# Performance work log

Hardware: AMD Instinct MI355X
Metric: run time of the kernel (lower is better)

Reference implementation:

```python
import jax, jax.numpy as jnp
import numpy as np

WS = 7            # window size (fixed by RelativeEmbedding default)
EMBED = 96
HEADS = 3
BATCH = 64
SIDE = 56         # height = width = sqrt(3136)
NEG_INF = float('-inf')


def _rel_bias_from_table(b_np):
    # Faithful reproduction of RelativeEmbedding.__init__ indexing quirks:
    # x = arange(1, ws+1, 1/ws) -> 49 floats; diffs truncated toward zero (.int())
    x = np.arange(1, WS + 1, 1.0 / WS, dtype=np.float32)
    xi = np.trunc(x[None, :] - x[:, None]).astype(np.int64)  # in [-6, 6]
    y = np.concatenate([np.arange(1, WS + 1)] * WS)
    yi = (y[None, :] - y[:, None]).astype(np.int64)          # in [-6, 6]
    n = 2 * WS - 1  # 13; emulate torch negative indexing with mod
    return b_np[xi % n, yi % n]  # (49, 49)


def _shift_masks():
    m = WS * (WS // 2)  # 21
    row_mask = np.zeros((WS * WS, WS * WS), dtype=np.float32)
    row_mask[-m:, :-m] = NEG_INF
    row_mask[:-m, -m:] = NEG_INF
    # rearrange '(r w1) (c w2) -> (w1 r) (w2 c)'
    col_mask = row_mask.reshape(WS, WS, WS, WS).transpose(1, 0, 3, 2).reshape(WS * WS, WS * WS)
    return jnp.asarray(row_mask), jnp.asarray(col_mask)


def setup_inputs() -> dict:
    key = jax.random.key(0)
    k1, k2, k3, k4, k5, k6 = jax.random.split(key, 6)
    x = jax.random.normal(k1, (BATCH, SIDE * SIDE, EMBED), dtype=jnp.float32)
    w1 = jax.random.normal(k2, (EMBED, 3 * EMBED), dtype=jnp.float32) * 0.02
    b1 = jnp.zeros((3 * EMBED,), dtype=jnp.float32)
    w2 = jax.random.normal(k3, (EMBED, EMBED), dtype=jnp.float32) * 0.02
    b2 = jnp.zeros((EMBED,), dtype=jnp.float32)
    b_table = np.asarray(jax.random.normal(k4, (2 * WS - 1, 2 * WS - 1), dtype=jnp.float32))
    rel_bias = jnp.asarray(_rel_bias_from_table(b_table))  # (49, 49), non-trainable
    return {"x": x, "w1": w1, "b1": b1, "w2": w2, "b2": b2, "rel_bias": rel_bias}


def reference(x, w1, b1, w2, b2, rel_bias):
    Bz, N, C = x.shape
    side = SIDE
    H = HEADS
    E = C // H          # head dim = 32
    nh = side // WS     # 8 windows per side

    qkv = x @ w1 + b1                                   # (B, N, 3C)
    # 'b (h w) (c K) -> b h w c K' with K=3 fastest-varying
    qkv = qkv.reshape(Bz, side, side, C, 3)
    # shifted-window roll; note (-7)//2 == -4 in Python (faithful to source)
    qkv = jnp.roll(qkv, ((-WS) // 2, (-WS) // 2), axis=(1, 2))
    # 'b (h m1) (w m2) (H E) K -> b H h w (m1 m2) E K'
    qkv = qkv.reshape(Bz, nh, WS, nh, WS, H, E, 3)
    qkv = qkv.transpose(0, 5, 1, 3, 2, 4, 6, 7).reshape(Bz, H, nh, nh, WS * WS, E, 3)
    q, k, v = qkv[..., 0], qkv[..., 1], qkv[..., 2]

    scale = jnp.sqrt(jnp.float32(E))
    att = jnp.einsum('bHhwme,bHhwne->bHhwmn', q, k) / scale  # (B,H,8,8,49,49)
    att = att + rel_bias

    row_mask, col_mask = _shift_masks()
    att = att.at[:, :, -1, :].add(row_mask)   # last window row
    att = att.at[:, :, :, -1].add(col_mask)   # last window column

    p = jax.nn.softmax(att, axis=-1)
    out = jnp.einsum('bHhwmn,bHhwne->bHhwme', p, v)          # (B,H,8,8,49,32)

    # 'b H h w (m1 m2) E -> b (h m1) (w m2) (H E)'
    out = out.reshape(Bz, H, nh, nh, WS, WS, E)
    out = out.transpose(0, 2, 4, 3, 5, 1, 6).reshape(Bz, side, side, C)
    # reverse roll uses +(7//2) == +3 (faithful asymmetry in the source)
    out = jnp.roll(out, (WS // 2, WS // 2), axis=(1, 2))
    out = out.reshape(Bz, N, C)
    return out @ w2 + b2
```

## Files before the change

kernel.cpp:

```cpp
#include <hip/hip_runtime.h>
#include <hip/hip_fp16.h>

typedef _Float16 half8_t __attribute__((ext_vector_type(8)));
typedef _Float16 half4_t __attribute__((ext_vector_type(4)));
typedef float f32x4 __attribute__((ext_vector_type(4)));
typedef unsigned int u32x4 __attribute__((ext_vector_type(4)));

#define WS_W2T 55296
#define WS_B1P 73728
#define WS_TBL 74880

__global__ __launch_bounds__(256) void swin_prep_kernel(
    const float* __restrict__ w1, const float* __restrict__ b1,
    const float* __restrict__ w2, const float* __restrict__ relb,
    _Float16* __restrict__ w1T, _Float16* __restrict__ w2T,
    float* __restrict__ b1p, float* __restrict__ tblP)
{
    int idx = blockIdx.x * 256 + threadIdx.x;
    const float L2E = 1.4426950408889634f;
    const float qs2 = 0.17677669529663687f * L2E;
    if (idx < 27648) {
        int jp = idx / 96, k = idx % 96;
        float v;
        if (jp < 96) {
            int f = jp >> 4, m = jp & 15;
            int cq = (f >> 1) * 32 + (m >> 2) * 8 + (f & 1) * 4 + (m & 3);
            v = w1[k * 288 + cq * 3] * qs2;
        } else {
            int jo = (jp % 96) * 3 + (jp / 96);
            v = w1[k * 288 + jo];
        }
        w1T[idx] = (_Float16)v;
    } else if (idx < 36864) {
        int i2 = idx - 27648;
        int n = i2 / 96, k = i2 % 96;
        w2T[i2] = (_Float16)w2[k * 96 + n];
    } else if (idx < 37152) {
        int jp = idx - 36864;
        float v = b1[(jp % 96) * 3 + (jp / 96)];
        if (jp < 96) v *= qs2;
        b1p[jp] = v;
    } else if (idx < 53536) {
        int t = idx - 37152;
        int vv = t >> 12, q = (t >> 6) & 63, c = t & 63;
        int i = c >> 4, m = c & 15;
        int k = (i >> 1) * 32 + (m >> 2) * 8 + (i & 1) * 4 + (m & 3);
        float val = -1e30f;
        if (q < 49 && k < 49) {
            val = relb[q * 49 + k] * L2E;
            if ((vv & 1) && ((q >= 28) != (k >= 28))) val = -1e30f;
            if ((vv & 2) && (((q % 7) >= 4) != ((k % 7) >= 4))) val = -1e30f;
        }
        tblP[t] = val;
    }
}

__device__ __forceinline__ unsigned int pack2h(float a, float b) {
    union { _Float16 h[2]; unsigned int u; } p;
    p.h[0] = (_Float16)a; p.h[1] = (_Float16)b;
    return p.u;
}

__global__ __launch_bounds__(256, 4) void swin_attn_kernel(
    const float* __restrict__ x,
    const _Float16* __restrict__ w1T,
    const _Float16* __restrict__ w2T,
    const float* __restrict__ b1p,
    const float* __restrict__ b2,
    const float* __restrict__ tblP,
    float* __restrict__ out)
{
    __shared__ __align__(16) char smem[27136];
    _Float16* Kb = (_Float16*)smem;
    _Float16* Vt = (_Float16*)(smem + 13312);
    _Float16* Xs = Kb;

    const int tid = threadIdx.x;
    const int wv = tid >> 6, lane = tid & 63;
    const int lr = lane & 15, lg = lane >> 4;

    const int gid = blockIdx.x;
    const int b = gid >> 6, wh = (gid >> 3) & 7, ww = gid & 7;
    const f32x4 fz = {0.f, 0.f, 0.f, 0.f};

    {
        const int p = tid >> 2, sub = tid & 3;
        const float* xrow = nullptr;
        if (p < 49) {
            const int m1 = p / 7, m2 = p % 7;
            int rr = wh * 7 + m1 + 4; if (rr >= 56) rr -= 56;
            int cc = ww * 7 + m2 + 4; if (cc >= 56) cc -= 56;
            xrow = x + ((size_t)b * 3136 + rr * 56 + cc) * 96;
        }
        #pragma unroll
        for (int j = 0; j < 6; ++j) {
            const int e = sub * 24 + j * 4;
            half4_t hv = {(_Float16)0.f, (_Float16)0.f, (_Float16)0.f, (_Float16)0.f};
            if (p < 49) {
                const float4 v = *(const float4*)(xrow + e);
                hv[0] = (_Float16)v.x; hv[1] = (_Float16)v.y;
                hv[2] = (_Float16)v.z; hv[3] = (_Float16)v.w;
            }
            *(half4_t*)(Xs + p * 104 + e) = hv;
        }
    }
    __syncthreads();

    half8_t xa[4][3], xq[3];
    #pragma unroll
    for (int mt = 0; mt < 4; ++mt)
        #pragma unroll
        for (int kt = 0; kt < 3; ++kt)
            xa[mt][kt] = *(const half8_t*)(Xs + (mt * 16 + lr) * 104 + kt * 32 + lg * 8);
    #pragma unroll
    for (int kt = 0; kt < 3; ++kt)
        xq[kt] = *(const half8_t*)(Xs + (wv * 16 + lr) * 104 + kt * 32 + lg * 8);
    __syncthreads();

    #pragma unroll 1
    for (int t = 0; t < 3; ++t) {
        const int nt = 6 + wv + 4 * t;
        half8_t bf[3];
        #pragma unroll
        for (int kt = 0; kt < 3; ++kt)
            bf[kt] = *(const half8_t*)(w1T + (nt * 16 + lr) * 96 + kt * 32 + lg * 8);
        const float bv = b1p[nt * 16 + lr];
        #pragma unroll
        for (int mt = 0; mt < 4; ++mt) {
            f32x4 acc = fz;
            #pragma unroll
            for (int kt = 0; kt < 3; ++kt)
                acc = __builtin_amdgcn_mfma_f32_16x16x32_f16(xa[mt][kt], bf[kt], acc, 0, 0, 0);
            if (nt < 12) {
                const int kc = ((nt - 6) * 16 + lr) ^ ((lg & 1) << 4);
                #pragma unroll
                for (int r = 0; r < 4; ++r) {
                    const int krow = ((mt >> 1) * 2 + (lg & 1)) * 16
                                   + ((mt * 2 + (lg >> 1)) & 3) * 4 + r;
                    Kb[krow * 104 + kc] = (_Float16)(acc[r] + bv);
                }
            } else {
                const int nv = nt - 12;
                const int hh = nv >> 1, eta = nv & 1;
                const int vrow = hh * 32 + ((lr >> 2) & 1) * 16
                               + (((eta << 1) + (lr >> 3)) & 3) * 4 + (lr & 3);
                half4_t hv;
                #pragma unroll
                for (int r = 0; r < 4; ++r) hv[r] = (_Float16)(acc[r] + bv);
                *(half4_t*)(Vt + vrow * 72 + mt * 16 + lg * 4) = hv;
            }
        }
    }

    unsigned int qpk[3][4];
    #pragma unroll
    for (int f = 0; f < 6; ++f) {
        f32x4 acc = fz;
        #pragma unroll
        for (int kt = 0; kt < 3; ++kt) {
            half8_t af = *(const half8_t*)(w1T + (f * 16 + lr) * 96 + kt * 32 + lg * 8);
            acc = __builtin_amdgcn_mfma_f32_16x16x32_f16(af, xq[kt], acc, 0, 0, 0);
        }
        const float4 bq = *(const float4*)(b1p + (f >> 1) * 32 + lg * 8 + (f & 1) * 4);
        qpk[f >> 1][(f & 1) * 2 + 0] = pack2h(acc[0] + bq.x, acc[1] + bq.y);
        qpk[f >> 1][(f & 1) * 2 + 1] = pack2h(acc[2] + bq.z, acc[3] + bq.w);
    }
    __syncthreads();

    f32x4 tv[4];
    {
        const int q = wv * 16 + lr;
        #pragma unroll
        for (int i = 0; i < 4; ++i)
            tv[i] = *(const f32x4*)(tblP
                    + ((wh == 7) ? 4096 : 0) + ((ww == 7) ? 8192 : 0)
                    + q * 64 + i * 16 + lg * 4);
    }

    f32x4 accO[6];
    #pragma unroll
    for (int i = 0; i < 6; ++i) accO[i] = fz;

    #pragma unroll
    for (int h = 0; h < 3; ++h) {
        const u32x4 qd = {qpk[h][0], qpk[h][1], qpk[h][2], qpk[h][3]};
        const half8_t qv = __builtin_bit_cast(half8_t, qd);

        f32x4 s[4];
        #pragma unroll
        for (int i = 0; i < 4; ++i) {
            const int col = (h * 32 + lg * 8) ^ ((i & 1) << 4);
            half8_t kf = *(const half8_t*)(Kb + (i * 16 + lr) * 104 + col);
            s[i] = __builtin_amdgcn_mfma_f32_16x16x32_f16(kf, qv, fz, 0, 0, 0);
        }
        float sum = 0.f;
        #pragma unroll
        for (int i = 0; i < 4; ++i)
            #pragma unroll
            for (int r = 0; r < 4; ++r) {
                const float e = exp2f(s[i][r] + tv[i][r]);
                s[i][r] = e; sum += e;
            }
        const u32x4 p0 = {pack2h(s[0][0], s[0][1]), pack2h(s[0][2], s[0][3]),
                          pack2h(s[1][0], s[1][1]), pack2h(s[1][2], s[1][3])};
        const u32x4 p1 = {pack2h(s[2][0], s[2][1]), pack2h(s[2][2], s[2][3]),
                          pack2h(s[3][0], s[3][1]), pack2h(s[3][2], s[3][3])};
        const half8_t pf0 = __builtin_bit_cast(half8_t, p0);
        const half8_t pf1 = __builtin_bit_cast(half8_t, p1);
        sum += __shfl_xor(sum, 16);
        sum += __shfl_xor(sum, 32);
        f32x4 o0 = fz, o1 = fz;
        {
            half8_t vf00 = *(const half8_t*)(Vt + (h * 32 + lr) * 72 + lg * 8);
            half8_t vf01 = *(const half8_t*)(Vt + (h * 32 + lr) * 72 + 32 + lg * 8);
            half8_t vf10 = *(const half8_t*)(Vt + (h * 32 + 16 + lr) * 72 + lg * 8);
            half8_t vf11 = *(const half8_t*)(Vt + (h * 32 + 16 + lr) * 72 + 32 + lg * 8);
            o0 = __builtin_amdgcn_mfma_f32_16x16x32_f16(vf00, pf0, o0, 0, 0, 0);
            o0 = __builtin_amdgcn_mfma_f32_16x16x32_f16(vf01, pf1, o0, 0, 0, 0);
            o1 = __builtin_amdgcn_mfma_f32_16x16x32_f16(vf10, pf0, o1, 0, 0, 0);
            o1 = __builtin_amdgcn_mfma_f32_16x16x32_f16(vf11, pf1, o1, 0, 0, 0);
        }
        const float inv = 1.0f / sum;
        const u32x4 od = {pack2h(o0[0] * inv, o0[1] * inv), pack2h(o0[2] * inv, o0[3] * inv),
                          pack2h(o1[0] * inv, o1[1] * inv), pack2h(o1[2] * inv, o1[3] * inv)};
        const half8_t of = __builtin_bit_cast(half8_t, od);
        #pragma unroll
        for (int nt = 0; nt < 6; ++nt) {
            half8_t wf = *(const half8_t*)(w2T + (nt * 16 + lr) * 96 + h * 32 + lg * 8);
            accO[nt] = __builtin_amdgcn_mfma_f32_16x16x32_f16(of, wf, accO[nt], 0, 0, 0);
        }
    }

    float b2v[6];
    #pragma unroll
    for (int nt = 0; nt < 6; ++nt) b2v[nt] = b2[nt * 16 + lr];
    #pragma unroll
    for (int r = 0; r < 4; ++r) {
        const int row = wv * 16 + lg * 4 + r;
        if (row < 49) {
            const int m1 = row / 7, m2 = row % 7;
            int oi = wh * 7 + m1 + 3; if (oi >= 56) oi -= 56;
            int oj = ww * 7 + m2 + 3; if (oj >= 56) oj -= 56;
            float* op = out + ((size_t)b * 3136 + oi * 56 + oj) * 96;
            #pragma unroll
            for (int nt = 0; nt < 6; ++nt)
                op[nt * 16 + lr] = accO[nt][r] + b2v[nt];
        }
    }
}

extern "C" void kernel_launch(void* const* d_in, const int* in_sizes, int n_in,
                              void* d_out, int out_size, void* d_ws, size_t ws_size,
                              hipStream_t stream) {
    const float* x    = (const float*)d_in[0];
    const float* w1   = (const float*)d_in[1];
    const float* b1   = (const float*)d_in[2];
    const float* w2   = (const float*)d_in[3];
    const float* b2   = (const float*)d_in[4];
    const float* relb = (const float*)d_in[5];
    float* out = (float*)d_out;

    _Float16* w1T = (_Float16*)((char*)d_ws);
    _Float16* w2T = (_Float16*)((char*)d_ws + WS_W2T);
    float*    b1p = (float*)((char*)d_ws + WS_B1P);
    float*    tblP = (float*)((char*)d_ws + WS_TBL);

    swin_prep_kernel<<<210, 256, 0, stream>>>(w1, b1, w2, relb, w1T, w2T, b1p, tblP);
    swin_attn_kernel<<<4096, 256, 0, stream>>>(x, w1T, w2T, b1p, b2, tblP, out);
}
```

Before: 84.99 us.

## Process two windows per block with two waves each, doubling rows per wave

Each 256-thread block now handles two adjacent attention windows, with two waves per window. Each wave computes Q and the attention output for two 16-row query tiles, so every K/V fragment and w2 fragment read from LDS is reused twice. The bias/mask table is folded into the MFMA accumulator initialisation, and packing uses cvt_pkrtz. In exchange, LDS use doubles, occupancy drops to 3 blocks per CU, register pressure grows, and the grid is halved.

```diff
diff --git a/kernel.cpp b/kernel.cpp
--- a/kernel.cpp
+++ b/kernel.cpp
@@ -3,6 +3,7 @@
 
 typedef _Float16 half8_t __attribute__((ext_vector_type(8)));
 typedef _Float16 half4_t __attribute__((ext_vector_type(4)));
+typedef _Float16 half2_t __attribute__((ext_vector_type(2)));
 typedef float f32x4 __attribute__((ext_vector_type(4)));
 typedef unsigned int u32x4 __attribute__((ext_vector_type(4)));
 
@@ -60,8 +61,11 @@
     p.h[0] = (_Float16)a; p.h[1] = (_Float16)b;
     return p.u;
 }
-
-__global__ __launch_bounds__(256, 4) void swin_attn_kernel(
+__device__ __forceinline__ unsigned int pkrtz(float a, float b) {
+    return __builtin_bit_cast(unsigned int, __builtin_amdgcn_cvt_pkrtz(a, b));
+}
+
+__global__ __launch_bounds__(256, 3) void swin_attn_kernel(
     const float* __restrict__ x,
     const _Float16* __restrict__ w1T,
     const _Float16* __restrict__ w2T,
@@ -70,56 +74,60 @@
     const float* __restrict__ tblP,
     float* __restrict__ out)
 {
-    __shared__ __align__(16) char smem[27136];
-    _Float16* Kb = (_Float16*)smem;
-    _Float16* Vt = (_Float16*)(smem + 13312);
-    _Float16* Xs = Kb;
+    __shared__ __align__(16) char smem[54272];
 
     const int tid = threadIdx.x;
     const int wv = tid >> 6, lane = tid & 63;
     const int lr = lane & 15, lg = lane >> 4;
+    const int W = wv >> 1, wsub = wv & 1;
 
     const int gid = blockIdx.x;
-    const int b = gid >> 6, wh = (gid >> 3) & 7, ww = gid & 7;
+    const int b = gid >> 5, wh = (gid >> 2) & 7, jw = gid & 3;
+    const int ww = jw * 2 + W;
+
+    _Float16* Kb = (_Float16*)(smem + W * 13312);
+    _Float16* Vt = (_Float16*)(smem + 26624 + W * 13824);
     const f32x4 fz = {0.f, 0.f, 0.f, 0.f};
 
     {
-        const int p = tid >> 2, sub = tid & 3;
+        const int w0 = tid >> 7, p = (tid >> 1) & 63, sub = tid & 1;
+        _Float16* Xw = (_Float16*)(smem + w0 * 13312);
+        const int ww0 = jw * 2 + w0;
         const float* xrow = nullptr;
         if (p < 49) {
             const int m1 = p / 7, m2 = p % 7;
             int rr = wh * 7 + m1 + 4; if (rr >= 56) rr -= 56;
-            int cc = ww * 7 + m2 + 4; if (cc >= 56) cc -= 56;
+            int cc = ww0 * 7 + m2 + 4; if (cc >= 56) cc -= 56;
             xrow = x + ((size_t)b * 3136 + rr * 56 + cc) * 96;
         }
         #pragma unroll
-        for (int j = 0; j < 6; ++j) {
-            const int e = sub * 24 + j * 4;
+        for (int j = 0; j < 12; ++j) {
+            const int e = sub * 48 + j * 4;
             half4_t hv = {(_Float16)0.f, (_Float16)0.f, (_Float16)0.f, (_Float16)0.f};
             if (p < 49) {
                 const float4 v = *(const float4*)(xrow + e);
                 hv[0] = (_Float16)v.x; hv[1] = (_Float16)v.y;
                 hv[2] = (_Float16)v.z; hv[3] = (_Float16)v.w;
             }
-            *(half4_t*)(Xs + p * 104 + e) = hv;
+            *(half4_t*)(Xw + p * 104 + e) = hv;
         }
     }
     __syncthreads();
 
-    half8_t xa[4][3], xq[3];
-    #pragma unroll
-    for (int mt = 0; mt < 4; ++mt)
-        #pragma unroll
-        for (int kt = 0; kt < 3; ++kt)
-            xa[mt][kt] = *(const half8_t*)(Xs + (mt * 16 + lr) * 104 + kt * 32 + lg * 8);
-    #pragma unroll
-    for (int kt = 0; kt < 3; ++kt)
-        xq[kt] = *(const half8_t*)(Xs + (wv * 16 + lr) * 104 + kt * 32 + lg * 8);
+    half8_t xa[4][3];
+    {
+        const _Float16* Xs = (const _Float16*)(smem + W * 13312);
+        #pragma unroll
+        for (int mt = 0; mt < 4; ++mt)
+            #pragma unroll
+            for (int kt = 0; kt < 3; ++kt)
+                xa[mt][kt] = *(const half8_t*)(Xs + (mt * 16 + lr) * 104 + kt * 32 + lg * 8);
+    }
     __syncthreads();
 
-    #pragma unroll 1
-    for (int t = 0; t < 3; ++t) {
-        const int nt = 6 + wv + 4 * t;
+    #pragma unroll
+    for (int t = 0; t < 6; ++t) {
+        const int nt = 6 + wsub + 2 * t;
         half8_t bf[3];
         #pragma unroll
         for (int kt = 0; kt < 3; ++kt)
@@ -152,82 +160,94 @@
         }
     }
 
-    unsigned int qpk[3][4];
-    #pragma unroll
-    for (int f = 0; f < 6; ++f) {
-        f32x4 acc = fz;
-        #pragma unroll
-        for (int kt = 0; kt < 3; ++kt) {
-            half8_t af = *(const half8_t*)(w1T + (f * 16 + lr) * 96 + kt * 32 + lg * 8);
-            acc = __builtin_amdgcn_mfma_f32_16x16x32_f16(af, xq[kt], acc, 0, 0, 0);
-        }
-        const float4 bq = *(const float4*)(b1p + (f >> 1) * 32 + lg * 8 + (f & 1) * 4);
-        qpk[f >> 1][(f & 1) * 2 + 0] = pack2h(acc[0] + bq.x, acc[1] + bq.y);
-        qpk[f >> 1][(f & 1) * 2 + 1] = pack2h(acc[2] + bq.z, acc[3] + bq.w);
+    unsigned int qpk[2][3][4];
+    #pragma unroll
+    for (int g = 0; g < 2; ++g) {
+        #pragma unroll
+        for (int f = 0; f < 6; ++f) {
+            f32x4 acc = fz;
+            #pragma unroll
+            for (int kt = 0; kt < 3; ++kt) {
+                half8_t af = *(const half8_t*)(w1T + (f * 16 + lr) * 96 + kt * 32 + lg * 8);
+                acc = __builtin_amdgcn_mfma_f32_16x16x32_f16(af, xa[wsub * 2 + g][kt], acc, 0, 0, 0);
+            }
+            const float4 bq = *(const float4*)(b1p + (f >> 1) * 32 + lg * 8 + (f & 1) * 4);
+            qpk[g][f >> 1][(f & 1) * 2 + 0] = pack2h(acc[0] + bq.x, acc[1] + bq.y);
+            qpk[g][f >> 1][(f & 1) * 2 + 1] = pack2h(acc[2] + bq.z, acc[3] + bq.w);
+        }
     }
     __syncthreads();
 
-    f32x4 tv[4];
-    {
-        const int q = wv * 16 + lr;
-        #pragma unroll
-        for (int i = 0; i < 4; ++i)
-            tv[i] = *(const f32x4*)(tblP
-                    + ((wh == 7) ? 4096 : 0) + ((ww == 7) ? 8192 : 0)
-                    + q * 64 + i * 16 + lg * 4);
-    }
-
-    f32x4 accO[6];
-    #pragma unroll
-    for (int i = 0; i < 6; ++i) accO[i] = fz;
+    const float* tblv = tblP + ((wh == 7) ? 4096 : 0) + ((ww == 7) ? 8192 : 0);
+    f32x4 accO[2][6];
+    #pragma unroll
+    for (int g = 0; g < 2; ++g)
+        #pragma unroll
+        for (int i = 0; i < 6; ++i) accO[g][i] = fz;
 
     #pragma unroll
     for (int h = 0; h < 3; ++h) {
-        const u32x4 qd = {qpk[h][0], qpk[h][1], qpk[h][2], qpk[h][3]};
-        const half8_t qv = __builtin_bit_cast(half8_t, qd);
-
-        f32x4 s[4];
+        half8_t qv[2];
+        #pragma unroll
+        for (int g = 0; g < 2; ++g) {
+            const u32x4 qd = {qpk[g][h][0], qpk[g][h][1], qpk[g][h][2], qpk[g][h][3]};
+            qv[g] = __builtin_bit_cast(half8_t, qd);
+        }
+        f32x4 s[2][4];
         #pragma unroll
         for (int i = 0; i < 4; ++i) {
             const int col = (h * 32 + lg * 8) ^ ((i & 1) << 4);
             half8_t kf = *(const half8_t*)(Kb + (i * 16 + lr) * 104 + col);
-            s[i] = __builtin_amdgcn_mfma_f32_16x16x32_f16(kf, qv, fz, 0, 0, 0);
-        }
-        float sum = 0.f;
-        #pragma unroll
-        for (int i = 0; i < 4; ++i)
-            #pragma unroll
-            for (int r = 0; r < 4; ++r) {
-                const float e = exp2f(s[i][r] + tv[i][r]);
-                s[i][r] = e; sum += e;
-            }
-        const u32x4 p0 = {pack2h(s[0][0], s[0][1]), pack2h(s[0][2], s[0][3]),
-                          pack2h(s[1][0], s[1][1]), pack2h(s[1][2], s[1][3])};
-        const u32x4 p1 = {pack2h(s[2][0], s[2][1]), pack2h(s[2][2], s[2][3]),
-                          pack2h(s[3][0], s[3][1]), pack2h(s[3][2], s[3][3])};
-        const half8_t pf0 = __builtin_bit_cast(half8_t, p0);
-        const half8_t pf1 = __builtin_bit_cast(half8_t, p1);
-        sum += __shfl_xor(sum, 16);
-        sum += __shfl_xor(sum, 32);
-        f32x4 o0 = fz, o1 = fz;
-        {
-            half8_t vf00 = *(const half8_t*)(Vt + (h * 32 + lr) * 72 + lg * 8);
-            half8_t vf01 = *(const half8_t*)(Vt + (h * 32 + lr) * 72 + 32 + lg * 8);
-            half8_t vf10 = *(const half8_t*)(Vt + (h * 32 + 16 + lr) * 72 + lg * 8);
-            half8_t vf11 = *(const half8_t*)(Vt + (h * 32 + 16 + lr) * 72 + 32 + lg * 8);
-            o0 = __builtin_amdgcn_mfma_f32_16x16x32_f16(vf00, pf0, o0, 0, 0, 0);
-            o0 = __builtin_amdgcn_mfma_f32_16x16x32_f16(vf01, pf1, o0, 0, 0, 0);
-            o1 = __builtin_amdgcn_mfma_f32_16x16x32_f16(vf10, pf0, o1, 0, 0, 0);
-            o1 = __builtin_amdgcn_mfma_f32_16x16x32_f16(vf11, pf1, o1, 0, 0, 0);
-        }
-        const float inv = 1.0f / sum;
-        const u32x4 od = {pack2h(o0[0] * inv, o0[1] * inv), pack2h(o0[2] * inv, o0[3] * inv),
-                          pack2h(o1[0] * inv, o1[1] * inv), pack2h(o1[2] * inv, o1[3] * inv)};
-        const half8_t of = __builtin_bit_cast(half8_t, od);
+            #pragma unroll
+            for (int g = 0; g < 2; ++g) {
+                const f32x4 tvv = *(const f32x4*)(tblv + ((wsub * 2 + g) * 16 + lr) * 64
+                                                  + i * 16 + lg * 4);
+                s[g][i] = __builtin_amdgcn_mfma_f32_16x16x32_f16(kf, qv[g], tvv, 0, 0, 0);
+            }
+        }
+        float sum[2];
+        half8_t pf0[2], pf1[2];
+        #pragma unroll
+        for (int g = 0; g < 2; ++g) {
+            float sm = 0.f;
+            #pragma unroll
+            for (int i = 0; i < 4; ++i)
+                #pragma unroll
+                for (int r = 0; r < 4; ++r) {
+                    const float e = exp2f(s[g][i][r]);
+                    s[g][i][r] = e; sm += e;
+                }
+            const u32x4 p0 = {pkrtz(s[g][0][0], s[g][0][1]), pkrtz(s[g][0][2], s[g][0][3]),
+                              pkrtz(s[g][1][0], s[g][1][1]), pkrtz(s[g][1][2], s[g][1][3])};
+            const u32x4 p1 = {pkrtz(s[g][2][0], s[g][2][1]), pkrtz(s[g][2][2], s[g][2][3]),
+                              pkrtz(s[g][3][0], s[g][3][1]), pkrtz(s[g][3][2], s[g][3][3])};
+            pf0[g] = __builtin_bit_cast(half8_t, p0);
+            pf1[g] = __builtin_bit_cast(half8_t, p1);
+            sm += __shfl_xor(sm, 16);
+            sm += __shfl_xor(sm, 32);
+            sum[g] = sm;
+        }
+        half8_t vf00 = *(const half8_t*)(Vt + (h * 32 + lr) * 72 + lg * 8);
+        half8_t vf01 = *(const half8_t*)(Vt + (h * 32 + lr) * 72 + 32 + lg * 8);
+        half8_t vf10 = *(const half8_t*)(Vt + (h * 32 + 16 + lr) * 72 + lg * 8);
+        half8_t vf11 = *(const half8_t*)(Vt + (h * 32 + 16 + lr) * 72 + 32 + lg * 8);
+        half8_t of[2];
+        #pragma unroll
+        for (int g = 0; g < 2; ++g) {
+            f32x4 o0 = __builtin_amdgcn_mfma_f32_16x16x32_f16(vf00, pf0[g], fz, 0, 0, 0);
+            o0 = __builtin_amdgcn_mfma_f32_16x16x32_f16(vf01, pf1[g], o0, 0, 0, 0);
+            f32x4 o1 = __builtin_amdgcn_mfma_f32_16x16x32_f16(vf10, pf0[g], fz, 0, 0, 0);
+            o1 = __builtin_amdgcn_mfma_f32_16x16x32_f16(vf11, pf1[g], o1, 0, 0, 0);
+            const float inv = 1.0f / sum[g];
+            const u32x4 od = {pack2h(o0[0] * inv, o0[1] * inv), pack2h(o0[2] * inv, o0[3] * inv),
+                              pack2h(o1[0] * inv, o1[1] * inv), pack2h(o1[2] * inv, o1[3] * inv)};
+            of[g] = __builtin_bit_cast(half8_t, od);
+        }
         #pragma unroll
         for (int nt = 0; nt < 6; ++nt) {
             half8_t wf = *(const half8_t*)(w2T + (nt * 16 + lr) * 96 + h * 32 + lg * 8);
-            accO[nt] = __builtin_amdgcn_mfma_f32_16x16x32_f16(of, wf, accO[nt], 0, 0, 0);
+            accO[0][nt] = __builtin_amdgcn_mfma_f32_16x16x32_f16(of[0], wf, accO[0][nt], 0, 0, 0);
+            accO[1][nt] = __builtin_amdgcn_mfma_f32_16x16x32_f16(of[1], wf, accO[1][nt], 0, 0, 0);
         }
     }
 
@@ -235,16 +255,19 @@
     #pragma unroll
     for (int nt = 0; nt < 6; ++nt) b2v[nt] = b2[nt * 16 + lr];
     #pragma unroll
-    for (int r = 0; r < 4; ++r) {
-        const int row = wv * 16 + lg * 4 + r;
-        if (row < 49) {
-            const int m1 = row / 7, m2 = row % 7;
-            int oi = wh * 7 + m1 + 3; if (oi >= 56) oi -= 56;
-            int oj = ww * 7 + m2 + 3; if (oj >= 56) oj -= 56;
-            float* op = out + ((size_t)b * 3136 + oi * 56 + oj) * 96;
-            #pragma unroll
-            for (int nt = 0; nt < 6; ++nt)
-                op[nt * 16 + lr] = accO[nt][r] + b2v[nt];
+    for (int g = 0; g < 2; ++g) {
+        #pragma unroll
+        for (int r = 0; r < 4; ++r) {
+            const int row = (wsub * 2 + g) * 16 + lg * 4 + r;
+            if (row < 49) {
+                const int m1 = row / 7, m2 = row % 7;
+                int oi = wh * 7 + m1 + 3; if (oi >= 56) oi -= 56;
+                int oj = ww * 7 + m2 + 3; if (oj >= 56) oj -= 56;
+                float* op = out + ((size_t)b * 3136 + oi * 56 + oj) * 96;
+                #pragma unroll
+                for (int nt = 0; nt < 6; ++nt)
+                    op[nt * 16 + lr] = accO[g][nt][r] + b2v[nt];
+            }
         }
     }
 }
@@ -260,11 +283,11 @@
     const float* relb = (const float*)d_in[5];
     float* out = (float*)d_out;
 
-    _Float16* w1T = (_Float16*)((char*)d_ws);
-    _Float16* w2T = (_Float16*)((char*)d_ws + WS_W2T);
-    float*    b1p = (float*)((char*)d_ws + WS_B1P);
+    _Float16* w1T  = (_Float16*)((char*)d_ws);
+    _Float16* w2T  = (_Float16*)((char*)d_ws + WS_W2T);
+    float*    b1p  = (float*)((char*)d_ws + WS_B1P);
     float*    tblP = (float*)((char*)d_ws + WS_TBL);
 
     swin_prep_kernel<<<210, 256, 0, stream>>>(w1, b1, w2, relb, w1T, w2T, b1p, tblP);
-    swin_attn_kernel<<<4096, 256, 0, stream>>>(x, w1T, w2T, b1p, b2, tblP, out);
-}
+    swin_attn_kernel<<<2048, 256, 0, stream>>>(x, w1T, w2T, b1p, b2, tblP, out);
+}
```

Result: slower. 105.4 us (+24.0%).

## Software-prefetch weight fragments and fold bias table into MFMA accumulator

Applied to the files above, without the earlier changes.

The K/V and Q projection loops now prefetch the next tile's w1T fragments before issuing the current MFMAs, so global loads overlap compute. The bias/mask table load moves before the barrier, and the table is used as the initial accumulator of the score MFMA, which removes a separate add. V and w2 fragments are loaded ahead of the softmax exp work. fp16 packing switches to the round-toward-zero pack instruction, and the softmax sum uses a tree reduction. The cost is higher register pressure under the 4-wave occupancy bound, plus slightly different rounding.

```diff
diff --git a/kernel.cpp b/kernel.cpp
--- a/kernel.cpp
+++ b/kernel.cpp
@@ -60,6 +60,9 @@
     p.h[0] = (_Float16)a; p.h[1] = (_Float16)b;
     return p.u;
 }
+__device__ __forceinline__ unsigned int pkrtz(float a, float b) {
+    return __builtin_bit_cast(unsigned int, __builtin_amdgcn_cvt_pkrtz(a, b));
+}
 
 __global__ __launch_bounds__(256, 4) void swin_attn_kernel(
     const float* __restrict__ x,
@@ -117,65 +120,88 @@
         xq[kt] = *(const half8_t*)(Xs + (wv * 16 + lr) * 104 + kt * 32 + lg * 8);
     __syncthreads();
 
-    #pragma unroll 1
-    for (int t = 0; t < 3; ++t) {
-        const int nt = 6 + wv + 4 * t;
-        half8_t bf[3];
-        #pragma unroll
-        for (int kt = 0; kt < 3; ++kt)
-            bf[kt] = *(const half8_t*)(w1T + (nt * 16 + lr) * 96 + kt * 32 + lg * 8);
-        const float bv = b1p[nt * 16 + lr];
-        #pragma unroll
-        for (int mt = 0; mt < 4; ++mt) {
+    {
+        half8_t bf0, bf1, bf2; float bv;
+        {
+            const int nt0 = 6 + wv;
+            bf0 = *(const half8_t*)(w1T + (nt0 * 16 + lr) * 96 + lg * 8);
+            bf1 = *(const half8_t*)(w1T + (nt0 * 16 + lr) * 96 + 32 + lg * 8);
+            bf2 = *(const half8_t*)(w1T + (nt0 * 16 + lr) * 96 + 64 + lg * 8);
+            bv = b1p[nt0 * 16 + lr];
+        }
+        #pragma unroll
+        for (int t = 0; t < 3; ++t) {
+            const int nt = 6 + wv + 4 * t;
+            half8_t nf0 = bf0, nf1 = bf1, nf2 = bf2; float nbv = bv;
+            if (t < 2) {
+                const int ntn = nt + 4;
+                nf0 = *(const half8_t*)(w1T + (ntn * 16 + lr) * 96 + lg * 8);
+                nf1 = *(const half8_t*)(w1T + (ntn * 16 + lr) * 96 + 32 + lg * 8);
+                nf2 = *(const half8_t*)(w1T + (ntn * 16 + lr) * 96 + 64 + lg * 8);
+                nbv = b1p[ntn * 16 + lr];
+            }
+            #pragma unroll
+            for (int mt = 0; mt < 4; ++mt) {
+                f32x4 acc = fz;
+                acc = __builtin_amdgcn_mfma_f32_16x16x32_f16(xa[mt][0], bf0, acc, 0, 0, 0);
+                acc = __builtin_amdgcn_mfma_f32_16x16x32_f16(xa[mt][1], bf1, acc, 0, 0, 0);
+                acc = __builtin_amdgcn_mfma_f32_16x16x32_f16(xa[mt][2], bf2, acc, 0, 0, 0);
+                if (nt < 12) {
+                    const int kc = ((nt - 6) * 16 + lr) ^ ((lg & 1) << 4);
+                    #pragma unroll
+                    for (int r = 0; r < 4; ++r) {
+                        const int krow = ((mt >> 1) * 2 + (lg & 1)) * 16
+                                       + ((mt * 2 + (lg >> 1)) & 3) * 4 + r;
+                        Kb[krow * 104 + kc] = (_Float16)(acc[r] + bv);
+                    }
+                } else {
+                    const int nv = nt - 12;
+                    const int hh = nv >> 1, eta = nv & 1;
+                    const int vrow = hh * 32 + ((lr >> 2) & 1) * 16
+                                   + (((eta << 1) + (lr >> 3)) & 3) * 4 + (lr & 3);
+                    half4_t hv;
+                    #pragma unroll
+                    for (int r = 0; r < 4; ++r) hv[r] = (_Float16)(acc[r] + bv);
+                    *(half4_t*)(Vt + vrow * 72 + mt * 16 + lg * 4) = hv;
+                }
+            }
+            bf0 = nf0; bf1 = nf1; bf2 = nf2; bv = nbv;
+        }
+    }
+
+    unsigned int qpk[3][4];
+    {
+        half8_t af0 = *(const half8_t*)(w1T + lr * 96 + lg * 8);
+        half8_t af1 = *(const half8_t*)(w1T + lr * 96 + 32 + lg * 8);
+        half8_t af2 = *(const half8_t*)(w1T + lr * 96 + 64 + lg * 8);
+        #pragma unroll
+        for (int f = 0; f < 6; ++f) {
+            half8_t n0 = af0, n1 = af1, n2 = af2;
+            if (f < 5) {
+                n0 = *(const half8_t*)(w1T + ((f + 1) * 16 + lr) * 96 + lg * 8);
+                n1 = *(const half8_t*)(w1T + ((f + 1) * 16 + lr) * 96 + 32 + lg * 8);
+                n2 = *(const half8_t*)(w1T + ((f + 1) * 16 + lr) * 96 + 64 + lg * 8);
+            }
             f32x4 acc = fz;
-            #pragma unroll
-            for (int kt = 0; kt < 3; ++kt)
-                acc = __builtin_amdgcn_mfma_f32_16x16x32_f16(xa[mt][kt], bf[kt], acc, 0, 0, 0);
-            if (nt < 12) {
-                const int kc = ((nt - 6) * 16 + lr) ^ ((lg & 1) << 4);
-                #pragma unroll
-                for (int r = 0; r < 4; ++r) {
-                    const int krow = ((mt >> 1) * 2 + (lg & 1)) * 16
-                                   + ((mt * 2 + (lg >> 1)) & 3) * 4 + r;
-                    Kb[krow * 104 + kc] = (_Float16)(acc[r] + bv);
-                }
-            } else {
-                const int nv = nt - 12;
-                const int hh = nv >> 1, eta = nv & 1;
-                const int vrow = hh * 32 + ((lr >> 2) & 1) * 16
-                               + (((eta << 1) + (lr >> 3)) & 3) * 4 + (lr & 3);
-                half4_t hv;
-                #pragma unroll
-                for (int r = 0; r < 4; ++r) hv[r] = (_Float16)(acc[r] + bv);
-                *(half4_t*)(Vt + vrow * 72 + mt * 16 + lg * 4) = hv;
-            }
-        }
-    }
-
-    unsigned int qpk[3][4];
-    #pragma unroll
-    for (int f = 0; f < 6; ++f) {
-        f32x4 acc = fz;
-        #pragma unroll
-        for (int kt = 0; kt < 3; ++kt) {
-            half8_t af = *(const half8_t*)(w1T + (f * 16 + lr) * 96 + kt * 32 + lg * 8);
-            acc = __builtin_amdgcn_mfma_f32_16x16x32_f16(af, xq[kt], acc, 0, 0, 0);
-        }
-        const float4 bq = *(const float4*)(b1p + (f >> 1) * 32 + lg * 8 + (f & 1) * 4);
-        qpk[f >> 1][(f & 1) * 2 + 0] = pack2h(acc[0] + bq.x, acc[1] + bq.y);
-        qpk[f >> 1][(f & 1) * 2 + 1] = pack2h(acc[2] + bq.z, acc[3] + bq.w);
+            acc = __builtin_amdgcn_mfma_f32_16x16x32_f16(af0, xq[0], acc, 0, 0, 0);
+            acc = __builtin_amdgcn_mfma_f32_16x16x32_f16(af1, xq[1], acc, 0, 0, 0);
+            acc = __builtin_amdgcn_mfma_f32_16x16x32_f16(af2, xq[2], acc, 0, 0, 0);
+            const float4 bq = *(const float4*)(b1p + (f >> 1) * 32 + lg * 8 + (f & 1) * 4);
+            qpk[f >> 1][(f & 1) * 2 + 0] = pack2h(acc[0] + bq.x, acc[1] + bq.y);
+            qpk[f >> 1][(f & 1) * 2 + 1] = pack2h(acc[2] + bq.z, acc[3] + bq.w);
+            af0 = n0; af1 = n1; af2 = n2;
+        }
+    }
+
+    f32x4 tv[4];
+    {
+        const float* tblv = tblP + ((wh == 7) ? 4096 : 0) + ((ww == 7) ? 8192 : 0)
+                          + (wv * 16 + lr) * 64 + lg * 4;
+        #pragma unroll
+        for (int i = 0; i < 4; ++i)
+            tv[i] = *(const f32x4*)(tblv + i * 16);
     }
     __syncthreads();
-
-    f32x4 tv[4];
-    {
-        const int q = wv * 16 + lr;
-        #pragma unroll
-        for (int i = 0; i < 4; ++i)
-            tv[i] = *(const f32x4*)(tblP
-                    + ((wh == 7) ? 4096 : 0) + ((ww == 7) ? 8192 : 0)
-                    + q * 64 + i * 16 + lg * 4);
-    }
 
     f32x4 accO[6];
     #pragma unroll
@@ -191,44 +217,45 @@
         for (int i = 0; i < 4; ++i) {
             const int col = (h * 32 + lg * 8) ^ ((i & 1) << 4);
             half8_t kf = *(const half8_t*)(Kb + (i * 16 + lr) * 104 + col);
-            s[i] = __builtin_amdgcn_mfma_f32_16x16x32_f16(kf, qv, fz, 0, 0, 0);
-        }
-        float sum = 0.f;
-        #pragma unroll
-        for (int i = 0; i < 4; ++i)
-            #pragma unroll
-            for (int r = 0; r < 4; ++r) {
-                const float e = exp2f(s[i][r] + tv[i][r]);
-                s[i][r] = e; sum += e;
-            }
-        const u32x4 p0 = {pack2h(s[0][0], s[0][1]), pack2h(s[0][2], s[0][3]),
-                          pack2h(s[1][0], s[1][1]), pack2h(s[1][2], s[1][3])};
-        const u32x4 p1 = {pack2h(s[2][0], s[2][1]), pack2h(s[2][2], s[2][3]),
-                          pack2h(s[3][0], s[3][1]), pack2h(s[3][2], s[3][3])};
+            s[i] = __builtin_amdgcn_mfma_f32_16x16x32_f16(kf, qv, tv[i], 0, 0, 0);
+        }
+        half8_t vf00 = *(const half8_t*)(Vt + (h * 32 + lr) * 72 + lg * 8);
+        half8_t vf01 = *(const half8_t*)(Vt + (h * 32 + lr) * 72 + 32 + lg * 8);
+        half8_t vf10 = *(const half8_t*)(Vt + (h * 32 + 16 + lr) * 72 + lg * 8);
+        half8_t vf11 = *(const half8_t*)(Vt + (h * 32 + 16 + lr) * 72 + 32 + lg * 8);
+        half8_t wf[6];
+        #pragma unroll
+        for (int nt = 0; nt < 6; ++nt)
+            wf[nt] = *(const half8_t*)(w2T + (nt * 16 + lr) * 96 + h * 32 + lg * 8);
+
+        float ps[4];
+        #pragma unroll
+        for (int i = 0; i < 4; ++i) {
+            float a0 = exp2f(s[i][0]), a1 = exp2f(s[i][1]);
+            float a2 = exp2f(s[i][2]), a3 = exp2f(s[i][3]);
+            s[i][0] = a0; s[i][1] = a1; s[i][2] = a2; s[i][3] = a3;
+            ps[i] = (a0 + a1) + (a2 + a3);
+        }
+        float sum = (ps[0] + ps[1]) + (ps[2] + ps[3]);
+        const u32x4 p0 = {pkrtz(s[0][0], s[0][1]), pkrtz(s[0][2], s[0][3]),
+                          pkrtz(s[1][0], s[1][1]), pkrtz(s[1][2], s[1][3])};
+        const u32x4 p1 = {pkrtz(s[2][0], s[2][1]), pkrtz(s[2][2], s[2][3]),
+                          pkrtz(s[3][0], s[3][1]), pkrtz(s[3][2], s[3][3])};
         const half8_t pf0 = __builtin_bit_cast(half8_t, p0);
         const half8_t pf1 = __builtin_bit_cast(half8_t, p1);
         sum += __shfl_xor(sum, 16);
         sum += __shfl_xor(sum, 32);
-        f32x4 o0 = fz, o1 = fz;
-        {
-            half8_t vf00 = *(const half8_t*)(Vt + (h * 32 + lr) * 72 + lg * 8);
-            half8_t vf01 = *(const half8_t*)(Vt + (h * 32 + lr) * 72 + 32 + lg * 8);
-            half8_t vf10 = *(const half8_t*)(Vt + (h * 32 + 16 + lr) * 72 + lg * 8);
-            half8_t vf11 = *(const half8_t*)(Vt + (h * 32 + 16 + lr) * 72 + 32 + lg * 8);
-            o0 = __builtin_amdgcn_mfma_f32_16x16x32_f16(vf00, pf0, o0, 0, 0, 0);
-            o0 = __builtin_amdgcn_mfma_f32_16x16x32_f16(vf01, pf1, o0, 0, 0, 0);
-            o1 = __builtin_amdgcn_mfma_f32_16x16x32_f16(vf10, pf0, o1, 0, 0, 0);
-            o1 = __builtin_amdgcn_mfma_f32_16x16x32_f16(vf11, pf1, o1, 0, 0, 0);
-        }
+        f32x4 o0 = __builtin_amdgcn_mfma_f32_16x16x32_f16(vf00, pf0, fz, 0, 0, 0);
+        o0 = __builtin_amdgcn_mfma_f32_16x16x32_f16(vf01, pf1, o0, 0, 0, 0);
+        f32x4 o1 = __builtin_amdgcn_mfma_f32_16x16x32_f16(vf10, pf0, fz, 0, 0, 0);
+        o1 = __builtin_amdgcn_mfma_f32_16x16x32_f16(vf11, pf1, o1, 0, 0, 0);
         const float inv = 1.0f / sum;
-        const u32x4 od = {pack2h(o0[0] * inv, o0[1] * inv), pack2h(o0[2] * inv, o0[3] * inv),
-                          pack2h(o1[0] * inv, o1[1] * inv), pack2h(o1[2] * inv, o1[3] * inv)};
+        const u32x4 od = {pkrtz(o0[0] * inv, o0[1] * inv), pkrtz(o0[2] * inv, o0[3] * inv),
+                          pkrtz(o1[0] * inv, o1[1] * inv), pkrtz(o1[2] * inv, o1[3] * inv)};
         const half8_t of = __builtin_bit_cast(half8_t, od);
         #pragma unroll
-        for (int nt = 0; nt < 6; ++nt) {
-            half8_t wf = *(const half8_t*)(w2T + (nt * 16 + lr) * 96 + h * 32 + lg * 8);
-            accO[nt] = __builtin_amdgcn_mfma_f32_16x16x32_f16(of, wf, accO[nt], 0, 0, 0);
-        }
+        for (int nt = 0; nt < 6; ++nt)
+            accO[nt] = __builtin_amdgcn_mfma_f32_16x16x32_f16(of, wf[nt], accO[nt], 0, 0, 0);
     }
 
     float b2v[6];
@@ -260,9 +287,9 @@
     const float* relb = (const float*)d_in[5];
     float* out = (float*)d_out;
 
-    _Float16* w1T = (_Float16*)((char*)d_ws);
-    _Float16* w2T = (_Float16*)((char*)d_ws + WS_W2T);
-    float*    b1p = (float*)((char*)d_ws + WS_B1P);
+    _Float16* w1T  = (_Float16*)((char*)d_ws);
+    _Float16* w2T  = (_Float16*)((char*)d_ws + WS_W2T);
+    float*    b1p  = (float*)((char*)d_ws + WS_B1P);
     float*    tblP = (float*)((char*)d_ws + WS_TBL);
 
     swin_prep_kernel<<<210, 256, 0, stream>>>(w1, b1, w2, relb, w1T, w2T, b1p, tblP);
```

Measured after the change: 91.43 us. 1.08x slower.
